# Performance work log

Hardware: AMD Instinct MI355X
Metric: run time of the kernel (lower is better)

Reference implementation:

```python
import jax, jax.numpy as jnp
import numpy as np

B, T, C, V = 8, 2048, 1024, 32000


def setup_inputs() -> dict:
    key = jax.random.key(0)
    ks = jax.random.split(key, 12)
    s = 1.0 / np.sqrt(C)
    return {
        "input_tokens": jax.random.randint(ks[0], (B, T), 0, V),
        "xx_init": jnp.zeros((B, C), jnp.float32),
        "aa_init": jnp.zeros((B, C), jnp.float32),
        "bb_init": jnp.zeros((B, C), jnp.float32),
        "pp_init": jnp.zeros((B, C), jnp.float32),  # with aa=bb=0 this is equivalent to -inf init
        "emb": jax.random.normal(ks[1], (V, C), jnp.float32) * 0.02,
        "time_mix_k": jax.random.uniform(ks[2], (C,), jnp.float32),
        "time_mix_v": jax.random.uniform(ks[3], (C,), jnp.float32),
        "time_mix_r": jax.random.uniform(ks[4], (C,), jnp.float32),
        "time_decay": jax.random.normal(ks[5], (C,), jnp.float32) * 0.1,
        "time_first": jax.random.normal(ks[6], (C,), jnp.float32) * 0.1,
        "Wk": jax.random.normal(ks[7], (C, C), jnp.float32) * s,
        "Wv": jax.random.normal(ks[8], (C, C), jnp.float32) * s,
        "Wr": jax.random.normal(ks[9], (C, C), jnp.float32) * s,
        "Wo": jax.random.normal(ks[10], (C, C), jnp.float32) * s,
    }


def _wkv_scan(k, v, aa0, bb0, pp0, w, u):
    """Numerically-stable RWKV WKV recurrence.
    k, v: [T, B, C]; aa0/bb0/pp0: [B, C]; w (decay, negative), u (bonus): [C]."""
    def step(carry, kv):
        aa, bb, pp = carry
        kt, vt = kv
        ww = u + kt
        p = jnp.maximum(pp, ww)
        e1 = jnp.exp(pp - p)
        e2 = jnp.exp(ww - p)
        wkv = (e1 * aa + e2 * vt) / (e1 * bb + e2)
        ww2 = pp + w
        p2 = jnp.maximum(ww2, kt)
        e1b = jnp.exp(ww2 - p2)
        e2b = jnp.exp(kt - p2)
        return (e1b * aa + e2b * vt, e1b * bb + e2b, p2), wkv
    (aa, bb, pp), out = jax.lax.scan(step, (aa0, bb0, pp0), (k, v))
    return out, aa, bb, pp


def _forward(input_tokens, xx_init, aa_init, bb_init, pp_init, emb,
             time_mix_k, time_mix_v, time_mix_r, time_decay, time_first,
             Wk, Wv, Wr, Wo):
    x = emb[input_tokens]                                   # [B, T, C]
    xprev = jnp.concatenate([xx_init[:, None, :], x[:, :-1]], axis=1)  # token shift
    xk = x * time_mix_k + xprev * (1.0 - time_mix_k)
    xv = x * time_mix_v + xprev * (1.0 - time_mix_v)
    xr = x * time_mix_r + xprev * (1.0 - time_mix_r)
    k = jnp.einsum("btc,dc->btd", xk, Wk)
    v = jnp.einsum("btc,dc->btd", xv, Wv)
    r = jax.nn.sigmoid(jnp.einsum("btc,dc->btd", xr, Wr))
    w = -jnp.exp(time_decay)                                # per-channel decay
    u = time_first
    wkv, _, _, _ = _wkv_scan(jnp.swapaxes(k, 0, 1), jnp.swapaxes(v, 0, 1),
                             aa_init, bb_init, pp_init, w, u)
    wkv = jnp.swapaxes(wkv, 0, 1)                           # [B, T, C]
    rwkv = jnp.einsum("btc,dc->btd", r * wkv, Wo)
    e1 = rwkv[:, -1]          # final-step state
    e2 = rwkv.mean(axis=1)    # time-averaged state
    hx = (e1 + e2) * 0.5
    return jnp.stack([hx, hx])  # (hx, cx) stacked -> [2, B, C]


def reference(input_tokens, xx_init, aa_init, bb_init, pp_init, emb,
              time_mix_k, time_mix_v, time_mix_r, time_decay, time_first,
              Wk, Wv, Wr, Wo):
    return _forward(input_tokens, xx_init, aa_init, bb_init, pp_init, emb,
                    time_mix_k, time_mix_v, time_mix_r, time_decay, time_first,
                    Wk, Wv, Wr, Wo)
```

## Files before the change

kernel.cpp:

```cpp
#include <hip/hip_runtime.h>

#define Bdim 8
#define Tdim 2048
#define Cdim 1024
#define NCH 128
#define CLEN 16
#define CG 32
#define BC (Bdim*Cdim)

typedef float floatx4 __attribute__((ext_vector_type(4)));
typedef _Float16 half8 __attribute__((ext_vector_type(8)));
typedef _Float16 half4v __attribute__((ext_vector_type(4)));

__device__ __forceinline__ void load16(const void* g, void* l) {
    __builtin_amdgcn_global_load_lds(
        (const __attribute__((address_space(1))) void*)g,
        (__attribute__((address_space(3))) void*)l, 16, 0, 0);
}

__global__ __launch_bounds__(256) void embed_mix3(const int* __restrict__ tokens,
                                                  const float* __restrict__ xx_init,
                                                  const float* __restrict__ emb,
                                                  const float* __restrict__ tmk,
                                                  const float* __restrict__ tmv,
                                                  const float* __restrict__ tmr,
                                                  _Float16* __restrict__ xk,
                                                  _Float16* __restrict__ xv,
                                                  _Float16* __restrict__ xr) {
    int row = blockIdx.x;
    int b = row >> 11;
    int t = row & (Tdim - 1);
    const float* cur = emb + (size_t)tokens[row] * Cdim;
    const float* prv = (t == 0) ? (xx_init + (size_t)b * Cdim)
                                : (emb + (size_t)tokens[row - 1] * Cdim);
    int c = threadIdx.x * 4;
    float4 cf4 = *reinterpret_cast<const float4*>(cur + c);
    float4 pf4 = *reinterpret_cast<const float4*>(prv + c);
    float4 mk = *reinterpret_cast<const float4*>(tmk + c);
    float4 mv = *reinterpret_cast<const float4*>(tmv + c);
    float4 mr = *reinterpret_cast<const float4*>(tmr + c);
    float cf[4] = {cf4.x, cf4.y, cf4.z, cf4.w};
    float pf[4] = {pf4.x, pf4.y, pf4.z, pf4.w};
    float mkf[4] = {mk.x, mk.y, mk.z, mk.w};
    float mvf[4] = {mv.x, mv.y, mv.z, mv.w};
    float mrf[4] = {mr.x, mr.y, mr.z, mr.w};
    half4v hk, hv, hr;
    #pragma unroll
    for (int j = 0; j < 4; j++) {
        hk[j] = (_Float16)(mkf[j] * cf[j] + (1.0f - mkf[j]) * pf[j]);
        hv[j] = (_Float16)(mvf[j] * cf[j] + (1.0f - mvf[j]) * pf[j]);
        hr[j] = (_Float16)(mrf[j] * cf[j] + (1.0f - mrf[j]) * pf[j]);
    }
    size_t o = (size_t)row * Cdim + c;
    *reinterpret_cast<half4v*>(xk + o) = hk;
    *reinterpret_cast<half4v*>(xv + o) = hv;
    *reinterpret_cast<half4v*>(xr + o) = hr;
}

__global__ __launch_bounds__(256) void wconv(const float* __restrict__ Wk,
                                             const float* __restrict__ Wv,
                                             const float* __restrict__ Wr,
                                             _Float16* __restrict__ Wh) {
    const float* W = blockIdx.y == 0 ? Wk : (blockIdx.y == 1 ? Wv : Wr);
    _Float16* dst = Wh + (size_t)blockIdx.y * Cdim * Cdim;
    int i = (blockIdx.x * 256 + threadIdx.x) * 4;
    float4 f = *reinterpret_cast<const float4*>(W + i);
    half4v h;
    h[0] = (_Float16)f.x; h[1] = (_Float16)f.y; h[2] = (_Float16)f.z; h[3] = (_Float16)f.w;
    *reinterpret_cast<half4v*>(dst + i) = h;
}

__global__ __launch_bounds__(256) void gemm_kvr(const _Float16* __restrict__ xk,
                                                const _Float16* __restrict__ xv,
                                                const _Float16* __restrict__ xr,
                                                const _Float16* __restrict__ Wh,
                                                _Float16* __restrict__ ko,
                                                _Float16* __restrict__ vo,
                                                _Float16* __restrict__ ro) {
    const int which = blockIdx.y;
    const _Float16* X = which == 0 ? xk : (which == 1 ? xv : xr);
    const _Float16* W = Wh + (size_t)which * Cdim * Cdim;
    _Float16* out     = which == 0 ? ko : (which == 1 ? vo : ro);

    const int lin = blockIdx.x;
    const int xcd = lin & 7;
    const int loc = lin >> 3;
    const int mt = xcd * 16 + (loc >> 3);
    const int nt = loc & 7;
    const int m0 = mt * 128;
    const int n0 = nt * 128;

    __shared__ _Float16 As[128 * 64];
    __shared__ _Float16 Bs[128 * 64];

    const int tid = threadIdx.x;
    const int lane = tid & 63;
    const int wave = tid >> 6;
    const int wm = (wave >> 1) * 64;
    const int wn = (wave & 1) * 64;
    const int lr = lane & 15;
    const int lk = lane >> 4;

    const _Float16* Asrc = X + (size_t)m0 * Cdim;
    const _Float16* Bsrc = W + (size_t)n0 * Cdim;

    floatx4 acc[4][4] = {};

    for (int k0 = 0; k0 < Cdim; k0 += 64) {
        #pragma unroll
        for (int i = 0; i < 4; i++) {
            int e = i * 256 + tid;
            int r = e >> 3;
            int cbp = e & 7;
            int cbl = cbp ^ (r & 7);
            load16(Asrc + (size_t)r * Cdim + k0 + cbl * 8, (char*)As + e * 16);
            load16(Bsrc + (size_t)r * Cdim + k0 + cbl * 8, (char*)Bs + e * 16);
        }
        __syncthreads();
        #pragma unroll
        for (int kk = 0; kk < 64; kk += 32) {
            const int kb_ = kk >> 3;
            half8 af[4], bf[4];
            #pragma unroll
            for (int mi = 0; mi < 4; mi++) {
                int r = wm + mi * 16 + lr;
                int cb = (kb_ + lk) ^ (r & 7);
                af[mi] = *reinterpret_cast<const half8*>(As + r * 64 + cb * 8);
            }
            #pragma unroll
            for (int ni = 0; ni < 4; ni++) {
                int r = wn + ni * 16 + lr;
                int cb = (kb_ + lk) ^ (r & 7);
                bf[ni] = *reinterpret_cast<const half8*>(Bs + r * 64 + cb * 8);
            }
            #pragma unroll
            for (int mi = 0; mi < 4; mi++)
                #pragma unroll
                for (int ni = 0; ni < 4; ni++)
                    acc[mi][ni] = __builtin_amdgcn_mfma_f32_16x16x32_f16(af[mi], bf[ni], acc[mi][ni], 0, 0, 0);
        }
        __syncthreads();
    }

    #pragma unroll
    for (int mi = 0; mi < 4; mi++) {
        #pragma unroll
        for (int ni = 0; ni < 4; ni++) {
            #pragma unroll
            for (int reg = 0; reg < 4; reg++) {
                int mm = m0 + wm + mi * 16 + (lane >> 4) * 4 + reg;
                int nn = n0 + wn + ni * 16 + (lane & 15);
                float v = acc[mi][ni][reg];
                if (which == 2) v = 1.0f / (1.0f + __expf(-v));
                out[(size_t)mm * Cdim + nn] = (_Float16)v;
            }
        }
    }
}

__global__ __launch_bounds__(1024) void wkv_fused(const _Float16* __restrict__ kb,
                                                  const _Float16* __restrict__ vb,
                                                  const _Float16* __restrict__ rb,
                                                  const float* __restrict__ tdecay,
                                                  const float* __restrict__ tfirst,
                                                  const float* __restrict__ aa_init,
                                                  const float* __restrict__ bb_init,
                                                  const float* __restrict__ pp_init,
                                                  float* __restrict__ z) {
    __shared__ float sa[NCH * CG];
    __shared__ float sbv[NCH * CG];
    __shared__ float sp[NCH * CG];
    __shared__ float ssum[NCH * CG];
    __shared__ float s2[8 * CG];
    __shared__ float syl[CG];

    const int b = blockIdx.x >> 5;
    const int cg = blockIdx.x & 31;
    const int tid = threadIdx.x;
    const int cl = tid & 7;
    const int j = tid >> 3;
    const int c0 = cg * CG + cl * 4;

    float4 td = *reinterpret_cast<const float4*>(tdecay + c0);
    float4 u4 = *reinterpret_cast<const float4*>(tfirst + c0);
    float w[4] = {-__expf(td.x), -__expf(td.y), -__expf(td.z), -__expf(td.w)};
    float u[4] = {u4.x, u4.y, u4.z, u4.w};

    const size_t base = ((size_t)(b * Tdim + j * CLEN)) * Cdim + c0;
    const _Float16* kp = kb + base;
    const _Float16* vp = vb + base;
    const _Float16* rp = rb + base;

    float aa[4], bb[4], pp[4];
    #pragma unroll
    for (int i = 0; i < 4; i++) { aa[i] = 0.0f; bb[i] = 0.0f; pp[i] = -1e30f; }
    #pragma unroll 4
    for (int t = 0; t < CLEN; t++) {
        half4v k4 = *reinterpret_cast<const half4v*>(kp + (size_t)t * Cdim);
        half4v v4 = *reinterpret_cast<const half4v*>(vp + (size_t)t * Cdim);
        #pragma unroll
        for (int i = 0; i < 4; i++) {
            float kt = (float)k4[i];
            float vt = (float)v4[i];
            float ww2 = pp[i] + w[i];
            float p2 = fmaxf(ww2, kt);
            float e1 = __expf(ww2 - p2);
            float e2 = __expf(kt - p2);
            aa[i] = e1 * aa[i] + e2 * vt;
            bb[i] = e1 * bb[i] + e2;
            pp[i] = p2;
        }
    }
    {
        int o = j * CG + cl * 4;
        #pragma unroll
        for (int i = 0; i < 4; i++) { sa[o + i] = aa[i]; sbv[o + i] = bb[i]; sp[o + i] = pp[i]; }
    }
    __syncthreads();

    if (tid < CG) {
        int ch = tid;
        float w1 = -__expf(tdecay[cg * CG + ch]);
        float wL = w1 * (float)CLEN;
        int gidx = b * Cdim + cg * CG + ch;
        float a = aa_init[gidx], bbv = bb_init[gidx], p = pp_init[gidx];
        for (int jj = 0; jj < NCH; jj++) {
            int o = jj * CG + ch;
            float ta = sa[o], tb = sbv[o], tp = sp[o];
            sa[o] = a; sbv[o] = bbv; sp[o] = p;
            float px = p + wL;
            float q = fmaxf(px, tp);
            float e1 = __expf(px - q);
            float e2 = __expf(tp - q);
            a = e1 * a + e2 * ta;
            bbv = e1 * bbv + e2 * tb;
            p = q;
        }
    }
    __syncthreads();

    float sum[4], ylv[4];
    {
        int o = j * CG + cl * 4;
        #pragma unroll
        for (int i = 0; i < 4; i++) {
            aa[i] = sa[o + i]; bb[i] = sbv[o + i]; pp[i] = sp[o + i];
            sum[i] = 0.0f; ylv[i] = 0.0f;
        }
    }
    #pragma unroll 4
    for (int t = 0; t < CLEN; t++) {
        half4v k4 = *reinterpret_cast<const half4v*>(kp + (size_t)t * Cdim);
        half4v v4 = *reinterpret_cast<const half4v*>(vp + (size_t)t * Cdim);
        half4v r4 = *reinterpret_cast<const half4v*>(rp + (size_t)t * Cdim);
        #pragma unroll
        for (int i = 0; i < 4; i++) {
            float kt = (float)k4[i];
            float vt = (float)v4[i];
            float rt = (float)r4[i];
            float ww = u[i] + kt;
            float p = fmaxf(pp[i], ww);
            float e1 = __expf(pp[i] - p);
            float e2 = __expf(ww - p);
            float wkv = (e1 * aa[i] + e2 * vt) / (e1 * bb[i] + e2);
            float y = rt * wkv;
            sum[i] += y;
            ylv[i] = y;
            float ww2 = pp[i] + w[i];
            float p2 = fmaxf(ww2, kt);
            float e1b = __expf(ww2 - p2);
            float e2b = __expf(kt - p2);
            aa[i] = e1b * aa[i] + e2b * vt;
            bb[i] = e1b * bb[i] + e2b;
            pp[i] = p2;
        }
    }
    {
        int o = j * CG + cl * 4;
        #pragma unroll
        for (int i = 0; i < 4; i++) ssum[o + i] = sum[i];
        if (j == NCH - 1) {
            #pragma unroll
            for (int i = 0; i < 4; i++) syl[cl * 4 + i] = ylv[i];
        }
    }
    __syncthreads();

    if (tid < 256) {
        int ch = tid & 31, s = tid >> 5;
        float acc = 0.0f;
        #pragma unroll
        for (int jj = 0; jj < 16; jj++) acc += ssum[(s * 16 + jj) * CG + ch];
        s2[s * CG + ch] = acc;
    }
    __syncthreads();
    if (tid < CG) {
        float acc = 0.0f;
        #pragma unroll
        for (int s = 0; s < 8; s++) acc += s2[s * CG + tid];
        z[(size_t)b * Cdim + cg * CG + tid] = 0.5f * (syl[tid] + acc * (1.0f / (float)Tdim));
    }
}

__global__ __launch_bounds__(256) void final_out(const float* __restrict__ z,
                                                 const float* __restrict__ Wo,
                                                 float* __restrict__ out) {
    int gw = (blockIdx.x * 256 + threadIdx.x) >> 6;
    int lane = threadIdx.x & 63;
    int b = gw >> 10;
    int d = gw & (Cdim - 1);
    const float4* zr = reinterpret_cast<const float4*>(z + (size_t)b * Cdim);
    const float4* wr = reinterpret_cast<const float4*>(Wo + (size_t)d * Cdim);
    float acc = 0.0f;
    #pragma unroll
    for (int s = 0; s < 4; s++) {
        float4 a = zr[lane + 64 * s];
        float4 w4 = wr[lane + 64 * s];
        acc += a.x * w4.x + a.y * w4.y + a.z * w4.z + a.w * w4.w;
    }
    #pragma unroll
    for (int off = 32; off > 0; off >>= 1) acc += __shfl_down(acc, off);
    if (lane == 0) {
        out[(size_t)b * Cdim + d] = acc;
        out[(size_t)BC + (size_t)b * Cdim + d] = acc;
    }
}

extern "C" void kernel_launch(void* const* d_in, const int* in_sizes, int n_in,
                              void* d_out, int out_size, void* d_ws, size_t ws_size,
                              hipStream_t stream) {
    const int*   tokens  = (const int*)d_in[0];
    const float* xx_init = (const float*)d_in[1];
    const float* aa_init = (const float*)d_in[2];
    const float* bb_init = (const float*)d_in[3];
    const float* pp_init = (const float*)d_in[4];
    const float* emb     = (const float*)d_in[5];
    const float* tmk     = (const float*)d_in[6];
    const float* tmv     = (const float*)d_in[7];
    const float* tmr     = (const float*)d_in[8];
    const float* tdecay  = (const float*)d_in[9];
    const float* tfirst  = (const float*)d_in[10];
    const float* Wk      = (const float*)d_in[11];
    const float* Wv      = (const float*)d_in[12];
    const float* Wr      = (const float*)d_in[13];
    const float* Wo      = (const float*)d_in[14];
    float* out = (float*)d_out;

    char* ws = (char*)d_ws;
    size_t off = 0;
    auto alloc = [&](size_t bytes) -> void* {
        void* p = ws + off;
        off += (bytes + 255) & ~(size_t)255;
        return p;
    };
    _Float16* xkb = (_Float16*)alloc((size_t)Bdim * Tdim * Cdim * 2);
    _Float16* xvb = (_Float16*)alloc((size_t)Bdim * Tdim * Cdim * 2);
    _Float16* xrb = (_Float16*)alloc((size_t)Bdim * Tdim * Cdim * 2);
    _Float16* kb = (_Float16*)alloc((size_t)Bdim * Tdim * Cdim * 2);
    _Float16* vb = (_Float16*)alloc((size_t)Bdim * Tdim * Cdim * 2);
    _Float16* rb = (_Float16*)alloc((size_t)Bdim * Tdim * Cdim * 2);
    _Float16* Wh = (_Float16*)alloc((size_t)3 * Cdim * Cdim * 2);
    float* zbuf = (float*)alloc((size_t)BC * 4);

    embed_mix3<<<Bdim * Tdim, 256, 0, stream>>>(tokens, xx_init, emb, tmk, tmv, tmr,
                                                xkb, xvb, xrb);
    wconv<<<dim3(1024, 3), 256, 0, stream>>>(Wk, Wv, Wr, Wh);
    gemm_kvr<<<dim3(1024, 3), 256, 0, stream>>>(xkb, xvb, xrb, Wh, kb, vb, rb);
    wkv_fused<<<Bdim * 32, 1024, 0, stream>>>(kb, vb, rb, tdecay, tfirst,
                                              aa_init, bb_init, pp_init, zbuf);
    final_out<<<(BC / 4), 256, 0, stream>>>(zbuf, Wo, out);
}
```

Before: 430.1 us.

## Write GEMM outputs in channel-group-major layout for contiguous WKV scan loads

```diff
diff --git a/kernel.cpp b/kernel.cpp
--- a/kernel.cpp
+++ b/kernel.cpp
@@ -70,18 +70,10 @@
     *reinterpret_cast<half4v*>(dst + i) = h;
 }
 
-__global__ __launch_bounds__(256) void gemm_kvr(const _Float16* __restrict__ xk,
-                                                const _Float16* __restrict__ xv,
-                                                const _Float16* __restrict__ xr,
-                                                const _Float16* __restrict__ Wh,
-                                                _Float16* __restrict__ ko,
-                                                _Float16* __restrict__ vo,
-                                                _Float16* __restrict__ ro) {
-    const int which = blockIdx.y;
-    const _Float16* X = which == 0 ? xk : (which == 1 ? xv : xr);
-    const _Float16* W = Wh + (size_t)which * Cdim * Cdim;
-    _Float16* out     = which == 0 ? ko : (which == 1 ? vo : ro);
-
+template<int WHICH>
+__global__ __launch_bounds__(256) void gemm_one(const _Float16* __restrict__ X,
+                                                const _Float16* __restrict__ Whh,
+                                                _Float16* __restrict__ outT) {
     const int lin = blockIdx.x;
     const int xcd = lin & 7;
     const int loc = lin >> 3;
@@ -90,8 +82,9 @@
     const int m0 = mt * 128;
     const int n0 = nt * 128;
 
-    __shared__ _Float16 As[128 * 64];
-    __shared__ _Float16 Bs[128 * 64];
+    __shared__ _Float16 S[128 * 128];
+    _Float16* As = S;
+    _Float16* Bs = S + 128 * 64;
 
     const int tid = threadIdx.x;
     const int lane = tid & 63;
@@ -102,7 +95,7 @@
     const int lk = lane >> 4;
 
     const _Float16* Asrc = X + (size_t)m0 * Cdim;
-    const _Float16* Bsrc = W + (size_t)n0 * Cdim;
+    const _Float16* Bsrc = Whh + (size_t)n0 * Cdim;
 
     floatx4 acc[4][4] = {};
 
@@ -148,25 +141,38 @@
         for (int ni = 0; ni < 4; ni++) {
             #pragma unroll
             for (int reg = 0; reg < 4; reg++) {
-                int mm = m0 + wm + mi * 16 + (lane >> 4) * 4 + reg;
-                int nn = n0 + wn + ni * 16 + (lane & 15);
+                int mm = wm + mi * 16 + (lane >> 4) * 4 + reg;
+                int nn = wn + ni * 16 + (lane & 15);
                 float v = acc[mi][ni][reg];
-                if (which == 2) v = 1.0f / (1.0f + __expf(-v));
-                out[(size_t)mm * Cdim + nn] = (_Float16)v;
+                if (WHICH == 2) v = 1.0f / (1.0f + __expf(-v));
+                int cb = nn >> 3, e = nn & 7;
+                S[mm * 128 + ((cb ^ (mm & 15)) << 3) + e] = (_Float16)v;
             }
         }
     }
-}
-
-__global__ __launch_bounds__(1024) void wkv_fused(const _Float16* __restrict__ kb,
-                                                  const _Float16* __restrict__ vb,
-                                                  const _Float16* __restrict__ rb,
-                                                  const float* __restrict__ tdecay,
-                                                  const float* __restrict__ tfirst,
-                                                  const float* __restrict__ aa_init,
-                                                  const float* __restrict__ bb_init,
-                                                  const float* __restrict__ pp_init,
-                                                  float* __restrict__ z) {
+    __syncthreads();
+    const int bb = m0 >> 11;
+    const int t0 = m0 & (Tdim - 1);
+    const int g0 = n0 >> 3;
+    #pragma unroll
+    for (int i = 0; i < 8; i++) {
+        int idx = i * 256 + tid;
+        int mm = idx & 127;
+        int cg8 = idx >> 7;
+        half8 val = *reinterpret_cast<const half8*>(&S[mm * 128 + ((cg8 ^ (mm & 15)) << 3)]);
+        *reinterpret_cast<half8*>(outT + (((size_t)bb * 128 + g0 + cg8) * Tdim + t0 + mm) * 8) = val;
+    }
+}
+
+__global__ __launch_bounds__(512) void wkv_fused(const _Float16* __restrict__ kT,
+                                                 const _Float16* __restrict__ vT,
+                                                 const _Float16* __restrict__ rT,
+                                                 const float* __restrict__ tdecay,
+                                                 const float* __restrict__ tfirst,
+                                                 const float* __restrict__ aa_init,
+                                                 const float* __restrict__ bb_init,
+                                                 const float* __restrict__ pp_init,
+                                                 float* __restrict__ z) {
     __shared__ float sa[NCH * CG];
     __shared__ float sbv[NCH * CG];
     __shared__ float sp[NCH * CG];
@@ -175,33 +181,37 @@
     __shared__ float syl[CG];
 
     const int b = blockIdx.x >> 5;
-    const int cg = blockIdx.x & 31;
+    const int cgrp = blockIdx.x & 31;
     const int tid = threadIdx.x;
-    const int cl = tid & 7;
-    const int j = tid >> 3;
-    const int c0 = cg * CG + cl * 4;
-
-    float4 td = *reinterpret_cast<const float4*>(tdecay + c0);
-    float4 u4 = *reinterpret_cast<const float4*>(tfirst + c0);
-    float w[4] = {-__expf(td.x), -__expf(td.y), -__expf(td.z), -__expf(td.w)};
-    float u[4] = {u4.x, u4.y, u4.z, u4.w};
-
-    const size_t base = ((size_t)(b * Tdim + j * CLEN)) * Cdim + c0;
-    const _Float16* kp = kb + base;
-    const _Float16* vp = vb + base;
-    const _Float16* rp = rb + base;
-
-    float aa[4], bb[4], pp[4];
-    #pragma unroll
-    for (int i = 0; i < 4; i++) { aa[i] = 0.0f; bb[i] = 0.0f; pp[i] = -1e30f; }
+    const int grp = tid & 3;
+    const int j = tid >> 2;
+    const int cg8 = cgrp * 4 + grp;
+    const int c0 = cg8 * 8;
+
+    float4 td0 = *reinterpret_cast<const float4*>(tdecay + c0);
+    float4 td1 = *reinterpret_cast<const float4*>(tdecay + c0 + 4);
+    float4 u0 = *reinterpret_cast<const float4*>(tfirst + c0);
+    float4 u1 = *reinterpret_cast<const float4*>(tfirst + c0 + 4);
+    float w[8] = {-__expf(td0.x), -__expf(td0.y), -__expf(td0.z), -__expf(td0.w),
+                  -__expf(td1.x), -__expf(td1.y), -__expf(td1.z), -__expf(td1.w)};
+    float u[8] = {u0.x, u0.y, u0.z, u0.w, u1.x, u1.y, u1.z, u1.w};
+
+    const size_t base = (((size_t)b * 128 + cg8) * Tdim + j * CLEN) * 8;
+    const _Float16* kp = kT + base;
+    const _Float16* vp = vT + base;
+    const _Float16* rp = rT + base;
+
+    float aa[8], bb[8], pp[8];
+    #pragma unroll
+    for (int i = 0; i < 8; i++) { aa[i] = 0.0f; bb[i] = 0.0f; pp[i] = -1e30f; }
     #pragma unroll 4
     for (int t = 0; t < CLEN; t++) {
-        half4v k4 = *reinterpret_cast<const half4v*>(kp + (size_t)t * Cdim);
-        half4v v4 = *reinterpret_cast<const half4v*>(vp + (size_t)t * Cdim);
-        #pragma unroll
-        for (int i = 0; i < 4; i++) {
-            float kt = (float)k4[i];
-            float vt = (float)v4[i];
+        half8 k8 = *reinterpret_cast<const half8*>(kp + t * 8);
+        half8 v8 = *reinterpret_cast<const half8*>(vp + t * 8);
+        #pragma unroll
+        for (int i = 0; i < 8; i++) {
+            float kt = (float)k8[i];
+            float vt = (float)v8[i];
             float ww2 = pp[i] + w[i];
             float p2 = fmaxf(ww2, kt);
             float e1 = __expf(ww2 - p2);
@@ -212,52 +222,52 @@
         }
     }
     {
-        int o = j * CG + cl * 4;
-        #pragma unroll
-        for (int i = 0; i < 4; i++) { sa[o + i] = aa[i]; sbv[o + i] = bb[i]; sp[o + i] = pp[i]; }
+        int o = j * CG + grp * 8;
+        #pragma unroll
+        for (int i = 0; i < 8; i++) { sa[o + i] = aa[i]; sbv[o + i] = bb[i]; sp[o + i] = pp[i]; }
     }
     __syncthreads();
 
     if (tid < CG) {
         int ch = tid;
-        float w1 = -__expf(tdecay[cg * CG + ch]);
+        float w1 = -__expf(tdecay[cgrp * CG + ch]);
         float wL = w1 * (float)CLEN;
-        int gidx = b * Cdim + cg * CG + ch;
-        float a = aa_init[gidx], bbv = bb_init[gidx], p = pp_init[gidx];
+        int gidx = b * Cdim + cgrp * CG + ch;
+        float a = aa_init[gidx], bv = bb_init[gidx], p = pp_init[gidx];
         for (int jj = 0; jj < NCH; jj++) {
             int o = jj * CG + ch;
             float ta = sa[o], tb = sbv[o], tp = sp[o];
-            sa[o] = a; sbv[o] = bbv; sp[o] = p;
+            sa[o] = a; sbv[o] = bv; sp[o] = p;
             float px = p + wL;
             float q = fmaxf(px, tp);
             float e1 = __expf(px - q);
             float e2 = __expf(tp - q);
             a = e1 * a + e2 * ta;
-            bbv = e1 * bbv + e2 * tb;
+            bv = e1 * bv + e2 * tb;
             p = q;
         }
     }
     __syncthreads();
 
-    float sum[4], ylv[4];
+    float sum[8], ylv[8];
     {
-        int o = j * CG + cl * 4;
-        #pragma unroll
-        for (int i = 0; i < 4; i++) {
+        int o = j * CG + grp * 8;
+        #pragma unroll
+        for (int i = 0; i < 8; i++) {
             aa[i] = sa[o + i]; bb[i] = sbv[o + i]; pp[i] = sp[o + i];
             sum[i] = 0.0f; ylv[i] = 0.0f;
         }
     }
     #pragma unroll 4
     for (int t = 0; t < CLEN; t++) {
-        half4v k4 = *reinterpret_cast<const half4v*>(kp + (size_t)t * Cdim);
-        half4v v4 = *reinterpret_cast<const half4v*>(vp + (size_t)t * Cdim);
-        half4v r4 = *reinterpret_cast<const half4v*>(rp + (size_t)t * Cdim);
-        #pragma unroll
-        for (int i = 0; i < 4; i++) {
-            float kt = (float)k4[i];
-            float vt = (float)v4[i];
-            float rt = (float)r4[i];
+        half8 k8 = *reinterpret_cast<const half8*>(kp + t * 8);
+        half8 v8 = *reinterpret_cast<const half8*>(vp + t * 8);
+        half8 r8 = *reinterpret_cast<const half8*>(rp + t * 8);
+        #pragma unroll
+        for (int i = 0; i < 8; i++) {
+            float kt = (float)k8[i];
+            float vt = (float)v8[i];
+            float rt = (float)r8[i];
             float ww = u[i] + kt;
             float p = fmaxf(pp[i], ww);
             float e1 = __expf(pp[i] - p);
@@ -276,12 +286,12 @@
         }
     }
     {
-        int o = j * CG + cl * 4;
-        #pragma unroll
-        for (int i = 0; i < 4; i++) ssum[o + i] = sum[i];
+        int o = j * CG + grp * 8;
+        #pragma unroll
+        for (int i = 0; i < 8; i++) ssum[o + i] = sum[i];
         if (j == NCH - 1) {
             #pragma unroll
-            for (int i = 0; i < 4; i++) syl[cl * 4 + i] = ylv[i];
+            for (int i = 0; i < 8; i++) syl[grp * 8 + i] = ylv[i];
         }
     }
     __syncthreads();
@@ -298,7 +308,7 @@
         float acc = 0.0f;
         #pragma unroll
         for (int s = 0; s < 8; s++) acc += s2[s * CG + tid];
-        z[(size_t)b * Cdim + cg * CG + tid] = 0.5f * (syl[tid] + acc * (1.0f / (float)Tdim));
+        z[(size_t)b * Cdim + cgrp * CG + tid] = 0.5f * (syl[tid] + acc * (1.0f / (float)Tdim));
     }
 }
 
@@ -365,8 +375,10 @@
     embed_mix3<<<Bdim * Tdim, 256, 0, stream>>>(tokens, xx_init, emb, tmk, tmv, tmr,
                                                 xkb, xvb, xrb);
     wconv<<<dim3(1024, 3), 256, 0, stream>>>(Wk, Wv, Wr, Wh);
-    gemm_kvr<<<dim3(1024, 3), 256, 0, stream>>>(xkb, xvb, xrb, Wh, kb, vb, rb);
-    wkv_fused<<<Bdim * 32, 1024, 0, stream>>>(kb, vb, rb, tdecay, tfirst,
-                                              aa_init, bb_init, pp_init, zbuf);
+    gemm_one<0><<<1024, 256, 0, stream>>>(xkb, Wh, kb);
+    gemm_one<1><<<1024, 256, 0, stream>>>(xvb, Wh + (size_t)Cdim * Cdim, vb);
+    gemm_one<2><<<1024, 256, 0, stream>>>(xrb, Wh + (size_t)2 * Cdim * Cdim, rb);
+    wkv_fused<<<Bdim * 32, 512, 0, stream>>>(kb, vb, rb, tdecay, tfirst,
+                                             aa_init, bb_init, pp_init, zbuf);
     final_out<<<(BC / 4), 256, 0, stream>>>(zbuf, Wo, out);
 }
```

Measured after the change: 486.1 us. 13.0% more time.
